# Kernel optimization log

Measured on AMD Instinct MI355X. Metric: run time of the kernel, lower is better.

## Reference

```python
import jax, jax.numpy as jnp
import numpy as np


def setup_inputs() -> dict:
    key = jax.random.key(0)
    k1, k2, k3, k4 = jax.random.split(key, 4)
    B, S, D, Y = 8, 2048, 512, 8921
    # xavier_uniform scale for [Y, D] weights
    lim = float(np.sqrt(6.0 / (Y + D)))
    x = jax.random.normal(k1, (B, S, D), dtype=jnp.float32)
    U_w = jax.random.uniform(k2, (Y, D), minval=-lim, maxval=lim, dtype=jnp.float32)
    final_w = jax.random.uniform(k3, (Y, D), minval=-lim, maxval=lim, dtype=jnp.float32)
    final_b = jax.random.normal(k4, (Y,), dtype=jnp.float32) * 0.02
    return {"x": x, "U_w": U_w, "final_w": final_w, "final_b": final_b}


def reference(x, U_w, final_w, final_b):
    # att: [B, Y, S] = U_w @ x^T
    att = jnp.einsum("yd,bsd->bys", U_w, x)
    alpha = jax.nn.softmax(att, axis=2)          # softmax over sequence
    m = jnp.einsum("bys,bsd->byd", alpha, x)      # per-label context [B, Y, D]
    y = jnp.einsum("yd,byd->by", final_w, m) + final_b  # [B, Y]
    return y
```

## Files before the change

kernel.cpp:

```cpp
#include <hip/hip_runtime.h>
#include <hip/hip_bf16.h>

constexpr int B_ = 8;
constexpr int S_ = 2048;
constexpr int D_ = 512;
constexpr int Y_ = 8921;
constexpr int MT_ = 70;
constexpr int SG_ = 4;

typedef __attribute__((ext_vector_type(8))) __bf16 bf16x8;
typedef __attribute__((ext_vector_type(4))) float f32x4;

__device__ __forceinline__ int swz_el(int row, int ksel8) {
  return row * 64 + ((ksel8 ^ row) & 7) * 8;
}

__global__ __launch_bounds__(256) void cvtW(const float* __restrict__ U,
                                            const float* __restrict__ F,
                                            __hip_bfloat16* __restrict__ wsW) {
  const int c = blockIdx.x * 256 + threadIdx.x;
  const int tile = c >> 11;
  const int row = (c >> 3) & 255;
  const int cs = c & 7;
  const int mt = tile >> 3, kt = tile & 7;
  const int ch = cs ^ (row & 7);
  const int g = row >> 5, h = (row >> 4) & 1, w = row & 15;
  const int y = mt * 128 + g * 16 + w;
  float4 f0 = {0.f, 0.f, 0.f, 0.f}, f1 = {0.f, 0.f, 0.f, 0.f};
  if (y < Y_) {
    const float* src = (h ? F : U) + (size_t)y * D_ + kt * 64 + ch * 8;
    f0 = reinterpret_cast<const float4*>(src)[0];
    f1 = reinterpret_cast<const float4*>(src)[1];
  }
  bf16x8 v;
  v[0] = (__bf16)f0.x; v[1] = (__bf16)f0.y; v[2] = (__bf16)f0.z; v[3] = (__bf16)f0.w;
  v[4] = (__bf16)f1.x; v[5] = (__bf16)f1.y; v[6] = (__bf16)f1.z; v[7] = (__bf16)f1.w;
  *reinterpret_cast<bf16x8*>(wsW + (size_t)c * 8) = v;
}

__global__ __launch_bounds__(256) void cvtX(const float* __restrict__ x,
                                            __hip_bfloat16* __restrict__ wsX) {
  const int c = blockIdx.x * 256 + threadIdx.x;
  const int tile = c >> 11;
  const int row = (c >> 3) & 255;
  const int cs = c & 7;
  const int b = tile >> 6, st = (tile >> 3) & 7, kt = tile & 7;
  const int ch = cs ^ (row & 7);
  const int s = st * 256 + row;
  const float* src = x + ((size_t)b * S_ + s) * D_ + kt * 64 + ch * 8;
  const float4 f0 = reinterpret_cast<const float4*>(src)[0];
  const float4 f1 = reinterpret_cast<const float4*>(src)[1];
  bf16x8 v;
  v[0] = (__bf16)f0.x; v[1] = (__bf16)f0.y; v[2] = (__bf16)f0.z; v[3] = (__bf16)f0.w;
  v[4] = (__bf16)f1.x; v[5] = (__bf16)f1.y; v[6] = (__bf16)f1.z; v[7] = (__bf16)f1.w;
  *reinterpret_cast<bf16x8*>(wsX + (size_t)c * 8) = v;
}

__global__ __launch_bounds__(256) void zeroLN(float* __restrict__ LN, int n) {
  const int i = blockIdx.x * 256 + threadIdx.x;
  if (i < n) LN[i] = 0.f;
}

__global__ __launch_bounds__(256) void combine(const float* __restrict__ Lg,
                                               const float* __restrict__ Ng,
                                               const float* __restrict__ fb,
                                               float* __restrict__ out) {
  const int y = blockIdx.x * 256 + threadIdx.x;
  const int b = blockIdx.y;
  if (y < Y_) out[(size_t)b * Y_ + y] = Ng[b * Y_ + y] / Lg[b * Y_ + y] + fb[y];
}

typedef const __attribute__((address_space(1))) void gv_t;
typedef __attribute__((address_space(3))) void lv_t;

__device__ __forceinline__ void gld_lds16(const void* g, void* l) {
  __builtin_amdgcn_global_load_lds((gv_t*)g, (lv_t*)l, 16, 0, 0);
}

__global__ __launch_bounds__(512, 2) void pool_main(
    const __hip_bfloat16* __restrict__ wsW, const __hip_bfloat16* __restrict__ wsX,
    float* __restrict__ Lg, float* __restrict__ Ng) {
  const int bid = blockIdx.x;
  const int b = bid & 7;
  const int r = bid >> 3;
  const int mt = r % MT_;
  const int sg = r / MT_;

  const int tid = threadIdx.x;
  const int lane = tid & 63;
  const int wid = tid >> 6;
  const int wm = wid >> 2;
  const int wn = wid & 3;
  const int l15 = lane & 15;
  const int l4 = lane >> 4;

  extern __shared__ __bf16 ldsA[];
  float* redL = reinterpret_cast<float*>(ldsA + 65536);
  float* redN = redL + 128;

  if (tid < 256) redL[tid] = 0.f;

  const __bf16* Wbase = (const __bf16*)wsW + (size_t)mt * 8 * 16384;
  const __bf16* Xbase = (const __bf16*)wsX + ((size_t)(b * 8 + sg * 2) * 8) * 16384;

  f32x4 acc[8][4];

  auto stageBoth = [&](int t1) {
    const int par = t1 & 1;
    const char* srcW = (const char*)(Wbase + (t1 & 7) * 16384) + wid * 4096 + lane * 16;
    const char* srcX = (const char*)(Xbase + (size_t)t1 * 16384) + wid * 4096 + lane * 16;
    char* dstW = (char*)ldsA + par * 32768 + wid * 4096;
    char* dstX = (char*)ldsA + 65536 + par * 32768 + wid * 4096;
#pragma unroll
    for (int i = 0; i < 4; ++i) gld_lds16(srcW + i * 1024, dstW + i * 1024);
#pragma unroll
    for (int i = 0; i < 4; ++i) gld_lds16(srcX + i * 1024, dstX + i * 1024);
  };

  auto fold = [&]() {
#pragma unroll
    for (int g = 0; g < 4; ++g)
#pragma unroll
      for (int q = 0; q < 4; ++q) {
        float l = 0.f, nn = 0.f;
#pragma unroll
        for (int n = 0; n < 4; ++n) {
          const float e = __expf(acc[2 * g][n][q]);
          l += e;
          nn = fmaf(e, acc[2 * g + 1][n][q], nn);
        }
#pragma unroll
        for (int mask = 1; mask <= 8; mask <<= 1) {
          l += __shfl_xor(l, mask);
          nn += __shfl_xor(nn, mask);
        }
        if (l15 == 0) {
          const int yl = wm * 64 + g * 16 + (l4 << 2) + q;
          atomicAdd(&redL[yl], l);
          atomicAdd(&redN[yl], nn);
        }
      }
  };

  auto zacc = [&]() {
#pragma unroll
    for (int m = 0; m < 8; ++m)
#pragma unroll
      for (int n = 0; n < 4; ++n) acc[m][n] = (f32x4){0.f, 0.f, 0.f, 0.f};
  };

  stageBoth(0);
  zacc();

  for (int t = 0; t < 16; ++t) {
    __syncthreads();
    if (t < 15) stageBoth(t + 1);

    const __bf16* A = ldsA + (t & 1) * 16384;
    const __bf16* Xl = ldsA + 32768 + (t & 1) * 16384;

    {
      bf16x8 xf[4], af[8];
#pragma unroll
      for (int n = 0; n < 4; ++n)
        xf[n] = *reinterpret_cast<const bf16x8*>(&Xl[swz_el(wn * 64 + n * 16 + l15, l4)]);
#pragma unroll
      for (int j = 0; j < 8; ++j)
        af[j] = *reinterpret_cast<const bf16x8*>(&A[swz_el(wm * 128 + j * 16 + l15, l4)]);
      __builtin_amdgcn_s_setprio(1);
#pragma unroll
      for (int j = 0; j < 8; ++j)
#pragma unroll
        for (int n = 0; n < 4; ++n)
          acc[j][n] = __builtin_amdgcn_mfma_f32_16x16x32_bf16(af[j], xf[n], acc[j][n], 0, 0, 0);
      __builtin_amdgcn_s_setprio(0);
    }
    {
      bf16x8 xf[4], af[8];
#pragma unroll
      for (int n = 0; n < 4; ++n)
        xf[n] = *reinterpret_cast<const bf16x8*>(&Xl[swz_el(wn * 64 + n * 16 + l15, 4 + l4)]);
#pragma unroll
      for (int j = 0; j < 8; ++j)
        af[j] = *reinterpret_cast<const bf16x8*>(&A[swz_el(wm * 128 + j * 16 + l15, 4 + l4)]);
      __builtin_amdgcn_s_setprio(1);
#pragma unroll
      for (int j = 0; j < 8; ++j)
#pragma unroll
        for (int n = 0; n < 4; ++n)
          acc[j][n] = __builtin_amdgcn_mfma_f32_16x16x32_bf16(af[j], xf[n], acc[j][n], 0, 0, 0);
      __builtin_amdgcn_s_setprio(0);
    }

    if (t == 7) { fold(); zacc(); }
  }
  fold();

  __syncthreads();
  if (tid < 128) {
    const int y = mt * 128 + tid;
    if (y < Y_) {
      atomicAdd(&Lg[(size_t)b * Y_ + y], redL[tid]);
      atomicAdd(&Ng[(size_t)b * Y_ + y], redN[tid]);
    }
  }
}

constexpr int FB_BY = 128, FB_BS = 64, FB_BK = 64;

__device__ __forceinline__ int fswz(int row, int k) {
  return row * FB_BK + ((((k >> 3) ^ row) & 7) << 3) + (k & 7);
}

template <int CHUNKS>
__device__ __forceinline__ void fb_stage(const float* __restrict__ gbase, int rstride,
                                         int maxrow, __bf16* lds, int tid) {
#pragma unroll
  for (int i = 0; i < CHUNKS / 256; ++i) {
    const int c = tid + 256 * i;
    const int row = c >> 3;
    const int ch = c & 7;
    float4 f0 = {0.f, 0.f, 0.f, 0.f}, f1 = {0.f, 0.f, 0.f, 0.f};
    if (row < maxrow) {
      const float4* p = reinterpret_cast<const float4*>(gbase + (size_t)row * rstride + ch * 8);
      f0 = p[0]; f1 = p[1];
    }
    bf16x8 v;
    v[0] = (__bf16)f0.x; v[1] = (__bf16)f0.y; v[2] = (__bf16)f0.z; v[3] = (__bf16)f0.w;
    v[4] = (__bf16)f1.x; v[5] = (__bf16)f1.y; v[6] = (__bf16)f1.z; v[7] = (__bf16)f1.w;
    *reinterpret_cast<bf16x8*>(&lds[fswz(row, ch * 8)]) = v;
  }
}

__global__ __launch_bounds__(256) void output_layer_fallback(
    const float* __restrict__ x, const float* __restrict__ Uw,
    const float* __restrict__ Fw, const float* __restrict__ fb,
    float* __restrict__ out) {
  const int b = blockIdx.y;
  const int y0 = blockIdx.x * FB_BY;
  const int tid = threadIdx.x;
  const int lane = tid & 63;
  const int w = tid >> 6;
  const int wm = (w >> 1) * 64, wn = (w & 1) * 32;
  __shared__ __bf16 sU[FB_BY * FB_BK], sF[FB_BY * FB_BK], sX[FB_BS * FB_BK];
  float Ls[4][4], Ns[4][4];
#pragma unroll
  for (int m = 0; m < 4; ++m)
#pragma unroll
    for (int q = 0; q < 4; ++q) { Ls[m][q] = 0.f; Ns[m][q] = 0.f; }
  const float* xb = x + (size_t)b * S_ * D_;
  const int umax = Y_ - y0;
  for (int s0 = 0; s0 < S_; s0 += FB_BS) {
    f32x4 accA[4][2] = {}, accP[4][2] = {};
    for (int k0 = 0; k0 < D_; k0 += FB_BK) {
      __syncthreads();
      fb_stage<FB_BY * 8>(Uw + (size_t)y0 * D_ + k0, D_, umax, sU, tid);
      fb_stage<FB_BY * 8>(Fw + (size_t)y0 * D_ + k0, D_, umax, sF, tid);
      fb_stage<FB_BS * 8>(xb + (size_t)s0 * D_ + k0, D_, FB_BS, sX, tid);
      __syncthreads();
#pragma unroll
      for (int kk = 0; kk < 2; ++kk) {
        const int kb = kk * 32 + (lane >> 4) * 8;
        bf16x8 bx[2];
#pragma unroll
        for (int n = 0; n < 2; ++n)
          bx[n] = *reinterpret_cast<const bf16x8*>(&sX[fswz(wn + n * 16 + (lane & 15), kb)]);
#pragma unroll
        for (int m = 0; m < 4; ++m) {
          const bf16x8 aU = *reinterpret_cast<const bf16x8*>(&sU[fswz(wm + m * 16 + (lane & 15), kb)]);
          const bf16x8 aF = *reinterpret_cast<const bf16x8*>(&sF[fswz(wm + m * 16 + (lane & 15), kb)]);
#pragma unroll
          for (int n = 0; n < 2; ++n) {
            accA[m][n] = __builtin_amdgcn_mfma_f32_16x16x32_bf16(aU, bx[n], accA[m][n], 0, 0, 0);
            accP[m][n] = __builtin_amdgcn_mfma_f32_16x16x32_bf16(aF, bx[n], accP[m][n], 0, 0, 0);
          }
        }
      }
    }
#pragma unroll
    for (int m = 0; m < 4; ++m)
#pragma unroll
      for (int n = 0; n < 2; ++n)
#pragma unroll
        for (int q = 0; q < 4; ++q) {
          const float e = __expf(accA[m][n][q]);
          Ls[m][q] += e;
          Ns[m][q] = fmaf(e, accP[m][n][q], Ns[m][q]);
        }
  }
  __syncthreads();
  float* redL = reinterpret_cast<float*>(sU);
  float* redN = reinterpret_cast<float*>(sF);
  for (int i = tid; i < FB_BY; i += 256) { redL[i] = 0.f; redN[i] = 0.f; }
  __syncthreads();
#pragma unroll
  for (int m = 0; m < 4; ++m)
#pragma unroll
    for (int q = 0; q < 4; ++q) {
      float l = Ls[m][q], nn = Ns[m][q];
#pragma unroll
      for (int mask = 1; mask <= 8; mask <<= 1) {
        l += __shfl_xor(l, mask);
        nn += __shfl_xor(nn, mask);
      }
      if ((lane & 15) == 0) {
        const int yl = wm + m * 16 + ((lane >> 4) << 2) + q;
        atomicAdd(&redL[yl], l);
        atomicAdd(&redN[yl], nn);
      }
    }
  __syncthreads();
  for (int i = tid; i < FB_BY; i += 256) {
    const int y = y0 + i;
    if (y < Y_) out[(size_t)b * Y_ + y] = redN[i] / redL[i] + fb[y];
  }
}

extern "C" void kernel_launch(void* const* d_in, const int* in_sizes, int n_in,
                              void* d_out, int out_size, void* d_ws,
                              size_t ws_size, hipStream_t stream) {
  const float* x = (const float*)d_in[0];
  const float* Uw = (const float*)d_in[1];
  const float* Fw = (const float*)d_in[2];
  const float* fb = (const float*)d_in[3];
  float* out = (float*)d_out;

  constexpr size_t W_EL = (size_t)MT_ * 8 * 16384;
  constexpr size_t X_EL = (size_t)B_ * 64 * 16384;
  constexpr size_t LN_FL = (size_t)2 * B_ * Y_;
  constexpr size_t WS_NEED = (W_EL + X_EL) * 2 + LN_FL * 4;
  constexpr int LDS_BYTES = 4 * 32768 + 1024;

  if (ws_size >= WS_NEED) {
    __hip_bfloat16* wsW = (__hip_bfloat16*)d_ws;
    __hip_bfloat16* wsX = wsW + W_EL;
    float* Lg = (float*)(wsX + X_EL);
    float* Ng = Lg + (size_t)B_ * Y_;

    cvtW<<<dim3((unsigned)(W_EL / 8 / 256)), dim3(256), 0, stream>>>(Uw, Fw, wsW);
    cvtX<<<dim3((unsigned)(X_EL / 8 / 256)), dim3(256), 0, stream>>>(x, wsX);
    zeroLN<<<dim3((unsigned)((LN_FL + 255) / 256)), dim3(256), 0, stream>>>(Lg, (int)LN_FL);

    hipFuncSetAttribute((const void*)pool_main,
                        hipFuncAttributeMaxDynamicSharedMemorySize, LDS_BYTES);
    pool_main<<<dim3(MT_ * B_ * SG_), dim3(512), LDS_BYTES, stream>>>(wsW, wsX, Lg, Ng);
    combine<<<dim3((Y_ + 255) / 256, B_), dim3(256), 0, stream>>>(Lg, Ng, fb, out);
  } else {
    output_layer_fallback<<<dim3(MT_, B_), dim3(256), 0, stream>>>(x, Uw, Fw, fb, out);
  }
}
```

Measured before the change: 347.2 us.

## Pre-arrange X in MFMA fragment order and load directly to registers

The X conversion kernel now writes bf16 X in the exact per-lane MFMA operand order, so the main kernel loads X fragments straight from global memory into registers instead of staging them through LDS. This halves LDS usage (only W is double-buffered) and removes the X LDS writes and reads. Block ordering also changes so that the four sequence groups of one label tile are adjacent, improving W reuse in cache. The trade-off is that global load latency for X is exposed inside the loop with no prefetch.

```diff
diff --git a/kernel.cpp b/kernel.cpp
--- a/kernel.cpp
+++ b/kernel.cpp
@@ -41,13 +41,16 @@
 __global__ __launch_bounds__(256) void cvtX(const float* __restrict__ x,
                                             __hip_bfloat16* __restrict__ wsX) {
   const int c = blockIdx.x * 256 + threadIdx.x;
-  const int tile = c >> 11;
-  const int row = (c >> 3) & 255;
-  const int cs = c & 7;
-  const int b = tile >> 6, st = (tile >> 3) & 7, kt = tile & 7;
-  const int ch = cs ^ (row & 7);
-  const int s = st * 256 + row;
-  const float* src = x + ((size_t)b * S_ + s) * D_ + kt * 64 + ch * 8;
+  const int lane = c & 63;
+  const int idx2 = (c >> 6) & 7;
+  const int wn = (c >> 9) & 3;
+  const int kt = (c >> 11) & 7;
+  const int st = (c >> 14) & 7;
+  const int b = (c >> 17) & 7;
+  const int n = idx2 >> 1, kk = idx2 & 1;
+  const int s = st * 256 + wn * 64 + n * 16 + (lane & 15);
+  const int k = kt * 64 + kk * 32 + (lane >> 4) * 8;
+  const float* src = x + ((size_t)b * S_ + s) * D_ + k;
   const float4 f0 = reinterpret_cast<const float4*>(src)[0];
   const float4 f1 = reinterpret_cast<const float4*>(src)[1];
   bf16x8 v;
@@ -83,8 +86,8 @@
   const int bid = blockIdx.x;
   const int b = bid & 7;
   const int r = bid >> 3;
-  const int mt = r % MT_;
-  const int sg = r / MT_;
+  const int sg = r & 3;
+  const int mt = r >> 2;
 
   const int tid = threadIdx.x;
   const int lane = tid & 63;
@@ -95,26 +98,22 @@
   const int l4 = lane >> 4;
 
   extern __shared__ __bf16 ldsA[];
-  float* redL = reinterpret_cast<float*>(ldsA + 65536);
+  float* redL = reinterpret_cast<float*>(ldsA + 32768);
   float* redN = redL + 128;
 
   if (tid < 256) redL[tid] = 0.f;
 
   const __bf16* Wbase = (const __bf16*)wsW + (size_t)mt * 8 * 16384;
-  const __bf16* Xbase = (const __bf16*)wsX + ((size_t)(b * 8 + sg * 2) * 8) * 16384;
+  const __bf16* xc = (const __bf16*)wsX +
+      ((size_t)(b * 8 + sg * 2) * 8) * 16384 + wn * 4096 + lane * 8;
 
   f32x4 acc[8][4];
 
-  auto stageBoth = [&](int t1) {
-    const int par = t1 & 1;
-    const char* srcW = (const char*)(Wbase + (t1 & 7) * 16384) + wid * 4096 + lane * 16;
-    const char* srcX = (const char*)(Xbase + (size_t)t1 * 16384) + wid * 4096 + lane * 16;
-    char* dstW = (char*)ldsA + par * 32768 + wid * 4096;
-    char* dstX = (char*)ldsA + 65536 + par * 32768 + wid * 4096;
-#pragma unroll
-    for (int i = 0; i < 4; ++i) gld_lds16(srcW + i * 1024, dstW + i * 1024);
-#pragma unroll
-    for (int i = 0; i < 4; ++i) gld_lds16(srcX + i * 1024, dstX + i * 1024);
+  auto stageW = [&](int t1) {
+    const char* src = (const char*)(Wbase + (t1 & 7) * 16384) + wid * 4096 + lane * 16;
+    char* dst = (char*)ldsA + (t1 & 1) * 32768 + wid * 4096;
+#pragma unroll
+    for (int i = 0; i < 4; ++i) gld_lds16(src + i * 1024, dst + i * 1024);
   };
 
   auto fold = [&]() {
@@ -149,21 +148,22 @@
       for (int n = 0; n < 4; ++n) acc[m][n] = (f32x4){0.f, 0.f, 0.f, 0.f};
   };
 
-  stageBoth(0);
+  stageW(0);
   zacc();
 
   for (int t = 0; t < 16; ++t) {
     __syncthreads();
-    if (t < 15) stageBoth(t + 1);
+    if (t < 15) stageW(t + 1);
+
+    bf16x8 xf[8];
+#pragma unroll
+    for (int f = 0; f < 8; ++f)
+      xf[f] = *reinterpret_cast<const bf16x8*>(xc + f * 512);
 
     const __bf16* A = ldsA + (t & 1) * 16384;
-    const __bf16* Xl = ldsA + 32768 + (t & 1) * 16384;
 
     {
-      bf16x8 xf[4], af[8];
-#pragma unroll
-      for (int n = 0; n < 4; ++n)
-        xf[n] = *reinterpret_cast<const bf16x8*>(&Xl[swz_el(wn * 64 + n * 16 + l15, l4)]);
+      bf16x8 af[8];
 #pragma unroll
       for (int j = 0; j < 8; ++j)
         af[j] = *reinterpret_cast<const bf16x8*>(&A[swz_el(wm * 128 + j * 16 + l15, l4)]);
@@ -172,14 +172,11 @@
       for (int j = 0; j < 8; ++j)
 #pragma unroll
         for (int n = 0; n < 4; ++n)
-          acc[j][n] = __builtin_amdgcn_mfma_f32_16x16x32_bf16(af[j], xf[n], acc[j][n], 0, 0, 0);
+          acc[j][n] = __builtin_amdgcn_mfma_f32_16x16x32_bf16(af[j], xf[2 * n], acc[j][n], 0, 0, 0);
       __builtin_amdgcn_s_setprio(0);
     }
     {
-      bf16x8 xf[4], af[8];
-#pragma unroll
-      for (int n = 0; n < 4; ++n)
-        xf[n] = *reinterpret_cast<const bf16x8*>(&Xl[swz_el(wn * 64 + n * 16 + l15, 4 + l4)]);
+      bf16x8 af[8];
 #pragma unroll
       for (int j = 0; j < 8; ++j)
         af[j] = *reinterpret_cast<const bf16x8*>(&A[swz_el(wm * 128 + j * 16 + l15, 4 + l4)]);
@@ -188,11 +185,12 @@
       for (int j = 0; j < 8; ++j)
 #pragma unroll
         for (int n = 0; n < 4; ++n)
-          acc[j][n] = __builtin_amdgcn_mfma_f32_16x16x32_bf16(af[j], xf[n], acc[j][n], 0, 0, 0);
+          acc[j][n] = __builtin_amdgcn_mfma_f32_16x16x32_bf16(af[j], xf[2 * n + 1], acc[j][n], 0, 0, 0);
       __builtin_amdgcn_s_setprio(0);
     }
 
     if (t == 7) { fold(); zacc(); }
+    xc += 16384;
   }
   fold();
 
@@ -329,7 +327,7 @@
   constexpr size_t X_EL = (size_t)B_ * 64 * 16384;
   constexpr size_t LN_FL = (size_t)2 * B_ * Y_;
   constexpr size_t WS_NEED = (W_EL + X_EL) * 2 + LN_FL * 4;
-  constexpr int LDS_BYTES = 4 * 32768 + 1024;
+  constexpr int LDS_BYTES = 2 * 32768 + 1024;
 
   if (ws_size >= WS_NEED) {
     __hip_bfloat16* wsW = (__hip_bfloat16*)d_ws;
```

Result: slower. 359.7 us (+3.6%).

## Interleave LDS fragment loads with MFMA phases and ping-pong wave barriers

Applied to the files above, without the earlier changes.

Restructures the main GEMM loop into four phases that each load a small slice of A fragments and run the matching MFMAs. The stage of the next tile is issued after the first fragment loads, and s_barrier calls bracket each MFMA burst so waves alternate between memory and compute. The single top-of-loop syncthreads is replaced by an explicit vmcnt(0) wait plus a barrier at the end of each iteration. This is meant to overlap LDS reads and global loads with matrix math, at the cost of more barriers per iteration and a tighter correctness dependence on the waitcnt placement.

```diff
diff --git a/kernel.cpp b/kernel.cpp
--- a/kernel.cpp
+++ b/kernel.cpp
@@ -150,46 +150,88 @@
   };
 
   stageBoth(0);
+  __syncthreads();
+  __builtin_amdgcn_sched_barrier(0);
   zacc();
 
   for (int t = 0; t < 16; ++t) {
-    __syncthreads();
-    if (t < 15) stageBoth(t + 1);
-
-    const __bf16* A = ldsA + (t & 1) * 16384;
-    const __bf16* Xl = ldsA + 32768 + (t & 1) * 16384;
-
+    const __bf16* A = ldsA + ((t & 1) << 14);
+    const __bf16* Xl = ldsA + 32768 + ((t & 1) << 14);
+    const bool has_next = (t < 15);
+
+    bf16x8 xf[2][4];
     {
-      bf16x8 xf[4], af[8];
-#pragma unroll
-      for (int n = 0; n < 4; ++n)
-        xf[n] = *reinterpret_cast<const bf16x8*>(&Xl[swz_el(wn * 64 + n * 16 + l15, l4)]);
-#pragma unroll
-      for (int j = 0; j < 8; ++j)
-        af[j] = *reinterpret_cast<const bf16x8*>(&A[swz_el(wm * 128 + j * 16 + l15, l4)]);
+      bf16x8 af[2][2];
+#pragma unroll
+      for (int j = 0; j < 2; ++j)
+#pragma unroll
+        for (int kk = 0; kk < 2; ++kk)
+          af[j][kk] = *reinterpret_cast<const bf16x8*>(
+              &A[swz_el(wm * 128 + j * 16 + l15, kk * 4 + l4)]);
+#pragma unroll
+      for (int kk = 0; kk < 2; ++kk)
+#pragma unroll
+        for (int n = 0; n < 4; ++n)
+          xf[kk][n] = *reinterpret_cast<const bf16x8*>(
+              &Xl[swz_el(wn * 64 + n * 16 + l15, kk * 4 + l4)]);
+      if (has_next) stageBoth(t + 1);
+      __builtin_amdgcn_s_barrier();
       __builtin_amdgcn_s_setprio(1);
 #pragma unroll
-      for (int j = 0; j < 8; ++j)
-#pragma unroll
-        for (int n = 0; n < 4; ++n)
-          acc[j][n] = __builtin_amdgcn_mfma_f32_16x16x32_bf16(af[j], xf[n], acc[j][n], 0, 0, 0);
+      for (int kk = 0; kk < 2; ++kk)
+#pragma unroll
+        for (int j = 0; j < 2; ++j)
+#pragma unroll
+          for (int n = 0; n < 4; ++n)
+            acc[j][n] = __builtin_amdgcn_mfma_f32_16x16x32_bf16(
+                af[j][kk], xf[kk][n], acc[j][n], 0, 0, 0);
       __builtin_amdgcn_s_setprio(0);
+      __builtin_amdgcn_s_barrier();
+    }
+#pragma unroll
+    for (int p = 1; p < 3; ++p) {
+      bf16x8 af[2][2];
+#pragma unroll
+      for (int j = 0; j < 2; ++j)
+#pragma unroll
+        for (int kk = 0; kk < 2; ++kk)
+          af[j][kk] = *reinterpret_cast<const bf16x8*>(
+              &A[swz_el(wm * 128 + (2 * p + j) * 16 + l15, kk * 4 + l4)]);
+      __builtin_amdgcn_s_barrier();
+      __builtin_amdgcn_s_setprio(1);
+#pragma unroll
+      for (int kk = 0; kk < 2; ++kk)
+#pragma unroll
+        for (int j = 0; j < 2; ++j)
+#pragma unroll
+          for (int n = 0; n < 4; ++n)
+            acc[2 * p + j][n] = __builtin_amdgcn_mfma_f32_16x16x32_bf16(
+                af[j][kk], xf[kk][n], acc[2 * p + j][n], 0, 0, 0);
+      __builtin_amdgcn_s_setprio(0);
+      __builtin_amdgcn_s_barrier();
     }
     {
-      bf16x8 xf[4], af[8];
-#pragma unroll
-      for (int n = 0; n < 4; ++n)
-        xf[n] = *reinterpret_cast<const bf16x8*>(&Xl[swz_el(wn * 64 + n * 16 + l15, 4 + l4)]);
-#pragma unroll
-      for (int j = 0; j < 8; ++j)
-        af[j] = *reinterpret_cast<const bf16x8*>(&A[swz_el(wm * 128 + j * 16 + l15, 4 + l4)]);
+      bf16x8 af[2][2];
+#pragma unroll
+      for (int j = 0; j < 2; ++j)
+#pragma unroll
+        for (int kk = 0; kk < 2; ++kk)
+          af[j][kk] = *reinterpret_cast<const bf16x8*>(
+              &A[swz_el(wm * 128 + (6 + j) * 16 + l15, kk * 4 + l4)]);
+      __builtin_amdgcn_s_barrier();
       __builtin_amdgcn_s_setprio(1);
 #pragma unroll
-      for (int j = 0; j < 8; ++j)
-#pragma unroll
-        for (int n = 0; n < 4; ++n)
-          acc[j][n] = __builtin_amdgcn_mfma_f32_16x16x32_bf16(af[j], xf[n], acc[j][n], 0, 0, 0);
+      for (int kk = 0; kk < 2; ++kk)
+#pragma unroll
+        for (int j = 0; j < 2; ++j)
+#pragma unroll
+          for (int n = 0; n < 4; ++n)
+            acc[6 + j][n] = __builtin_amdgcn_mfma_f32_16x16x32_bf16(
+                af[j][kk], xf[kk][n], acc[6 + j][n], 0, 0, 0);
       __builtin_amdgcn_s_setprio(0);
+      asm volatile("s_waitcnt vmcnt(0)" ::: "memory");
+      __builtin_amdgcn_s_barrier();
+      __builtin_amdgcn_sched_barrier(0);
     }
 
     if (t == 7) { fold(); zacc(); }
```

Measured after the change: 355.7 us. +2.4%, slower.
